# Kernel tuning notes

Hardware: AMD Instinct MI355X
Metric: run time of the kernel (lower is better)

## Reference

```python
import jax, jax.numpy as jnp
import numpy as np

B, L, C = 8, 2048, 512
R, H, DK = 256, 8, 64
MASK_NEG = -2.0**15 + 1.0


def setup_inputs() -> dict:
    key = jax.random.key(0)
    ks = jax.random.split(key, 9)
    s = 1.0 / np.sqrt(C)
    return {
        "qx": jax.random.normal(ks[0], (B, L, C), jnp.float32),
        "kx": jax.random.normal(ks[1], (B, L, C), jnp.float32),
        "vx": jax.random.normal(ks[2], (B, L, C), jnp.float32),
        "addLoss": jnp.zeros((), jnp.float32),
        "maskPAD": jnp.ones((B, L, L), jnp.bool_),
        "Wp": jax.random.normal(ks[3], (R, C), jnp.float32) * s,
        "WQ": jax.random.normal(ks[4], (H * DK, C), jnp.float32) * s,
        "WK": jax.random.normal(ks[5], (H * DK, C), jnp.float32) * s,
        "WV": jax.random.normal(ks[6], (H * DK, C), jnp.float32) * s,
        "WO": jax.random.normal(ks[7], (C, H * DK), jnp.float32) * (1.0 / np.sqrt(H * DK)),
    }


def reference(qx, kx, vx, addLoss, maskPAD, Wp, WQ, WK, WV, WO):
    # linearLevel == 'l1', dropout treated as identity (eval), training losses included
    b, l, c = qx.shape
    r = Wp.shape[0]
    offI = (1.0 - jnp.eye(r, dtype=qx.dtype))  # ones_minus_I, [r, r]

    pScore = jnp.einsum('blc,rc->blr', vx, Wp)                       # [B, L, r]
    pad = (maskPAD[:, 0] == 0)                                       # [B, L]
    pScore = jnp.where(pad[:, :, None], MASK_NEG, pScore)
    pAlpha = jnp.swapaxes(jax.nn.softmax(pScore, axis=-2), -1, -2)   # [B, r, L]
    pAlpha_ = jax.nn.softmax(pScore, axis=-1)                        # [B, L, r]

    addLoss = addLoss + jnp.mean((jnp.einsum('brl,bsl->brs', pAlpha, pAlpha) * offI) ** 2)

    qr = pAlpha @ qx                                                 # [B, r, C]
    kr = pAlpha @ kx
    vr = pAlpha @ vx

    queries = (qr @ WQ.T).reshape(b, r, H, DK).transpose(0, 2, 1, 3)  # [B, H, r, dk]
    keys = (kr @ WK.T).reshape(b, r, H, DK).transpose(0, 2, 1, 3)
    values = (vr @ WV.T).reshape(b, r, H, DK).transpose(0, 2, 1, 3)

    scores = jnp.einsum('bhrd,bhsd->bhrs', queries, keys) / jnp.asarray(np.sqrt(DK), qx.dtype)
    alpha = jax.nn.softmax(scores, axis=-1)                          # [B, H, r, r]
    addLoss = addLoss + jnp.mean(alpha * offI)

    z = alpha @ values                                               # [B, H, r, dk]
    z = z.transpose(0, 2, 1, 3).reshape(b, r, H * DK)
    z = z @ WO.T                                                     # [B, r, C]

    addLoss = addLoss + jnp.mean((jnp.einsum('blr,bls->brs', pAlpha_, pAlpha_) * offI) ** 2)
    z = pAlpha_ @ z                                                  # [B, L, C]
    return z, scores, addLoss
```

## Files before the change

### kernel.cpp

```cpp
#include <hip/hip_runtime.h>

#define B_  8
#define L_  2048
#define C_  512
#define R_  256
#define H_  8
#define DK_ 64
#define HD_ 512
#define MASK_NEG (-32767.0f)

typedef __attribute__((ext_vector_type(8))) short short8;
typedef __attribute__((ext_vector_type(8))) unsigned short ushort8;
typedef __attribute__((ext_vector_type(4))) unsigned short ushort4_t;
typedef __attribute__((ext_vector_type(4))) float f32x4;
typedef unsigned short u16;

__device__ inline u16 bf16_rne(float x) {
    unsigned u = __float_as_uint(x);
    return (u16)((u + 0x7FFFu + ((u >> 16) & 1u)) >> 16);
}
__device__ inline unsigned cvt_hl(float x) {
    u16 hh = bf16_rne(x);
    float hf = __uint_as_float(((unsigned)hh) << 16);
    u16 ll = bf16_rne(x - hf);
    return (unsigned)hh | ((unsigned)ll << 16);
}

struct Ptr3 { const void* p0; const void* p1; const void* p2; };

#define GLL16(g, l) __builtin_amdgcn_global_load_lds( \
    (const __attribute__((address_space(1))) void*)(g), \
    (__attribute__((address_space(3))) void*)(l), 16, 0, 0)

template<int BN, int AMODE, int BMODE, int EPI, bool TRIPLE, int NTERM = 3, int KSPLIT = 1>
__global__ __launch_bounds__(256) void gemm_pl(
    Ptr3 aH, Ptr3 aL, Ptr3 bH, Ptr3 bL, Ptr3 cH, Ptr3 cL,
    int K, int lda, int ldb, int ldc, int divz,
    long long ash, long long bsh, long long csh,
    long long asb, long long bsb, long long csb,
    long long ksa, long long ksb, long long ksc,
    float scale)
{
    constexpr int NF = BN / 32;
    constexpr int XA = (NTERM == 3) ? 64 : 1;
    constexpr int XB = (NTERM == 3) ? BN : 1;
    __shared__ u16 Ahs[64][40], Als[XA][40];
    __shared__ u16 Bhs[BN][40], Bls[XB][40];

    const int z  = blockIdx.z;
    const int zb = z / divz;
    const int rem = z - zb * divz;
    const int zh = rem / KSPLIT, ks = rem - zh * KSPLIT;
    const int Keff = K / KSPLIT;
    const void* avH = TRIPLE ? (zb == 0 ? aH.p0 : zb == 1 ? aH.p1 : aH.p2) : aH.p0;
    const void* avL = TRIPLE ? (zb == 0 ? aL.p0 : zb == 1 ? aL.p1 : aL.p2) : aL.p0;
    const void* bvH = TRIPLE ? (zb == 0 ? bH.p0 : zb == 1 ? bH.p1 : bH.p2) : bH.p0;
    const void* bvL = TRIPLE ? (zb == 0 ? bL.p0 : zb == 1 ? bL.p1 : bL.p2) : bL.p0;
    void* cvH = (void*)(TRIPLE ? (zb == 0 ? cH.p0 : zb == 1 ? cH.p1 : cH.p2) : cH.p0);
    void* cvL = (void*)(TRIPLE ? (zb == 0 ? cL.p0 : zb == 1 ? cL.p1 : cL.p2) : cL.p0);
    const long long ao = (TRIPLE ? 0 : (long long)zb * asb) + (long long)zh * ash + (long long)ks * ksa;
    const long long bo = (TRIPLE ? 0 : (long long)zb * bsb) + (long long)zh * bsh + (long long)ks * ksb;
    const long long co = (TRIPLE ? 0 : (long long)zb * csb) + (long long)zh * csh + (long long)ks * ksc;

    const u16*   AHg = (const u16*)avH + ao;
    const u16*   ALg = (const u16*)avL + ao;
    const u16*   BHg = (const u16*)bvH + bo;
    const u16*   BLg = (const u16*)bvL + bo;
    const float* Bfg = (const float*)bvH + bo;
    float* Cf  = (float*)cvH + co;
    u16*   CHg = (u16*)cvH + co;
    u16*   CLg = (u16*)cvL + co;

    const int m0 = blockIdx.y * 64, n0 = blockIdx.x * BN;
    const int tid = threadIdx.x;
    const int lane = tid & 63, w = tid >> 6;
    const int wrow = (w >> 1) * 32, wcol = (w & 1) * (BN / 2);
    const int l15 = lane & 15, lg = lane >> 4;

    f32x4 zero = {0.f, 0.f, 0.f, 0.f};
    f32x4 acc[2][NF];
    #pragma unroll
    for (int mf = 0; mf < 2; ++mf)
        #pragma unroll
        for (int nf = 0; nf < NF; ++nf) acc[mf][nf] = zero;

    for (int k0 = 0; k0 < Keff; k0 += 32) {
        {
            int row = tid >> 2, kc = (tid & 3) << 3;
            long long off = (long long)(m0 + row) * lda + (k0 + kc);
            *(ushort8*)&Ahs[row][kc] = *(const ushort8*)(AHg + off);
            if constexpr (NTERM == 3)
                *(ushort8*)&Als[row][kc] = *(const ushort8*)(ALg + off);
        }
        if (BMODE == 0) {
            #pragma unroll
            for (int t = tid; t < BN * 4; t += 256) {
                int row = t >> 2, kc = (t & 3) << 3;
                long long off = (long long)(n0 + row) * ldb + (k0 + kc);
                *(ushort8*)&Bhs[row][kc] = *(const ushort8*)(BHg + off);
                if constexpr (NTERM == 3)
                    *(ushort8*)&Bls[row][kc] = *(const ushort8*)(BLg + off);
            }
        } else {
            #pragma unroll
            for (int t = tid; t < BN * 4; t += 256) {
                int row = t >> 2, kc = (t & 3) << 3;
                const float* s = Bfg + (long long)(n0 + row) * ldb + (k0 + kc);
                float4 v0 = *(const float4*)s, v1 = *(const float4*)(s + 4);
                unsigned p0 = cvt_hl(v0.x), p1 = cvt_hl(v0.y), p2 = cvt_hl(v0.z), p3 = cvt_hl(v0.w);
                unsigned p4 = cvt_hl(v1.x), p5 = cvt_hl(v1.y), p6 = cvt_hl(v1.z), p7 = cvt_hl(v1.w);
                ushort8 h, l;
                h[0]=(u16)p0; h[1]=(u16)p1; h[2]=(u16)p2; h[3]=(u16)p3;
                h[4]=(u16)p4; h[5]=(u16)p5; h[6]=(u16)p6; h[7]=(u16)p7;
                l[0]=(u16)(p0>>16); l[1]=(u16)(p1>>16); l[2]=(u16)(p2>>16); l[3]=(u16)(p3>>16);
                l[4]=(u16)(p4>>16); l[5]=(u16)(p5>>16); l[6]=(u16)(p6>>16); l[7]=(u16)(p7>>16);
                *(ushort8*)&Bhs[row][kc] = h;
                if constexpr (NTERM == 3)
                    *(ushort8*)&Bls[row][kc] = l;
            }
        }
        __syncthreads();

        short8 a_h[2], a_l[2];
        a_h[0] = *(const short8*)&Ahs[wrow +      l15][lg * 8];
        a_h[1] = *(const short8*)&Ahs[wrow + 16 + l15][lg * 8];
        if constexpr (NTERM == 3) {
            a_l[0] = *(const short8*)&Als[wrow +      l15][lg * 8];
            a_l[1] = *(const short8*)&Als[wrow + 16 + l15][lg * 8];
        }
        #pragma unroll
        for (int nf = 0; nf < NF; ++nf) {
            short8 b_h = *(const short8*)&Bhs[wcol + nf * 16 + l15][lg * 8];
            if constexpr (NTERM == 3) {
                short8 b_l = *(const short8*)&Bls[wcol + nf * 16 + l15][lg * 8];
                #pragma unroll
                for (int mf = 0; mf < 2; ++mf) {
                    acc[mf][nf] = __builtin_amdgcn_mfma_f32_16x16x32_bf16(a_h[mf], b_h, acc[mf][nf], 0, 0, 0);
                    acc[mf][nf] = __builtin_amdgcn_mfma_f32_16x16x32_bf16(a_h[mf], b_l, acc[mf][nf], 0, 0, 0);
                    acc[mf][nf] = __builtin_amdgcn_mfma_f32_16x16x32_bf16(a_l[mf], b_h, acc[mf][nf], 0, 0, 0);
                }
            } else {
                #pragma unroll
                for (int mf = 0; mf < 2; ++mf)
                    acc[mf][nf] = __builtin_amdgcn_mfma_f32_16x16x32_bf16(a_h[mf], b_h, acc[mf][nf], 0, 0, 0);
            }
        }
        __syncthreads();
    }

    if (EPI == 0) {
        #pragma unroll
        for (int mf = 0; mf < 2; ++mf)
            #pragma unroll
            for (int nf = 0; nf < NF; ++nf) {
                int row = m0 + wrow + mf * 16 + lg * 4;
                int col = n0 + wcol + nf * 16 + l15;
                #pragma unroll
                for (int j = 0; j < 4; ++j)
                    Cf[(long long)(row + j) * ldc + col] = acc[mf][nf][j] * scale;
            }
    } else {
        #pragma unroll
        for (int mf = 0; mf < 2; ++mf)
            #pragma unroll
            for (int nf = 0; nf < NF; ++nf) {
                int row = m0 + wrow + mf * 16 + lg * 4;
                int col = n0 + wcol + nf * 16 + l15;
                #pragma unroll
                for (int j = 0; j < 4; ++j) {
                    unsigned p = cvt_hl(acc[mf][nf][j] * scale);
                    CHg[(long long)(row + j) * ldc + col] = (u16)p;
                    CLg[(long long)(row + j) * ldc + col] = (u16)(p >> 16);
                }
            }
    }
}

template<int EPI, bool TRIPLE, int NTERM, int KSPLIT>
__global__ __launch_bounds__(256) void gemm_gll(
    Ptr3 aH, Ptr3 aL, Ptr3 bH, Ptr3 bL, Ptr3 cH, Ptr3 cL,
    int K, int lda, int ldb, int ldc, int divz,
    long long ash, long long bsh, long long csh,
    long long ksa, long long ksb, long long ksc,
    float scale)
{
    constexpr int XA = (NTERM == 3) ? 128 : 1;
    __shared__ u16 Ahs[2][128][32];
    __shared__ u16 Bhs[2][128][32];
    __shared__ u16 Als[XA][32], Bls[XA][32];

    const int gx = gridDim.x, gy = gridDim.y;
    const int nwg = gx * gy * gridDim.z;
    int flat = blockIdx.x + gx * (blockIdx.y + gy * blockIdx.z);
    {
        int q = nwg >> 3;
        int xcd = flat & 7, idx = flat >> 3;
        flat = xcd * q + idx;
    }
    const int bx = flat % gx;
    const int by = (flat / gx) % gy;
    const int z  = flat / (gx * gy);

    const int zb = z / divz;
    const int rem = z - zb * divz;
    const int zh = rem / KSPLIT, ks = rem - zh * KSPLIT;
    const int Keff = K / KSPLIT;
    const void* avH = TRIPLE ? (zb == 0 ? aH.p0 : zb == 1 ? aH.p1 : aH.p2) : aH.p0;
    const void* avL = TRIPLE ? (zb == 0 ? aL.p0 : zb == 1 ? aL.p1 : aL.p2) : aL.p0;
    const void* bvH = TRIPLE ? (zb == 0 ? bH.p0 : zb == 1 ? bH.p1 : bH.p2) : bH.p0;
    const void* bvL = TRIPLE ? (zb == 0 ? bL.p0 : zb == 1 ? bL.p1 : bL.p2) : bL.p0;
    void* cvH = (void*)(TRIPLE ? (zb == 0 ? cH.p0 : zb == 1 ? cH.p1 : cH.p2) : cH.p0);
    void* cvL = (void*)(TRIPLE ? (zb == 0 ? cL.p0 : zb == 1 ? cL.p1 : cL.p2) : cL.p0);
    const long long ao = (long long)zh * ash + (long long)ks * ksa;
    const long long bo = (long long)zh * bsh + (long long)ks * ksb;
    const long long co = (long long)zh * csh + (long long)ks * ksc;

    const u16* AHg = (const u16*)avH + ao;
    const u16* ALg = (const u16*)avL + ao;
    const u16* BHg = (const u16*)bvH + bo;
    const u16* BLg = (const u16*)bvL + bo;
    float* Cf  = (float*)cvH + co;
    u16*   CHg = (u16*)cvH + co;
    u16*   CLg = (u16*)cvL + co;

    const int m0 = by * 128, n0 = bx * 128;
    const int tid = threadIdx.x;
    const int lane = tid & 63, w = tid >> 6;
    const int wrow = (w >> 1) * 64, wcol = (w & 1) * 64;
    const int l15 = lane & 15, lg = lane >> 4;

    f32x4 zero = {0.f, 0.f, 0.f, 0.f};
    f32x4 acc[4][4];
    #pragma unroll
    for (int mf = 0; mf < 4; ++mf)
        #pragma unroll
        for (int nf = 0; nf < 4; ++nf) acc[mf][nf] = zero;

    const int ric = lane >> 2;
    const int cc  = lane & 3;

    auto STAGE_HI = [&](int bufsel, int k0) {
        #pragma unroll
        for (int i = 0; i < 2; ++i) {
            int chunk = w * 2 + i;
            int row = chunk * 16 + ric;
            int gcol = ((cc ^ ((row >> 1) & 3)) << 3);
            GLL16(AHg + (long long)(m0 + row) * lda + (k0 + gcol), &Ahs[bufsel][chunk * 16][0]);
            GLL16(BHg + (long long)(n0 + row) * ldb + (k0 + gcol), &Bhs[bufsel][chunk * 16][0]);
        }
    };
    auto STAGE_LO = [&](int k0) {
        #pragma unroll
        for (int i = 0; i < 2; ++i) {
            int chunk = w * 2 + i;
            int row = chunk * 16 + ric;
            int gcol = ((cc ^ ((row >> 1) & 3)) << 3);
            GLL16(ALg + (long long)(m0 + row) * lda + (k0 + gcol), &Als[chunk * 16][0]);
            GLL16(BLg + (long long)(n0 + row) * ldb + (k0 + gcol), &Bls[chunk * 16][0]);
        }
    };

    const int nt = Keff / 32;
    int cur = 0;
    STAGE_HI(0, 0);

    for (int t = 0; t < nt; ++t) {
        if constexpr (NTERM == 3) STAGE_LO(t * 32);
        if (t + 1 < nt) {
            STAGE_HI(cur ^ 1, (t + 1) * 32);
            asm volatile("s_waitcnt vmcnt(4)" ::: "memory");
        } else {
            asm volatile("s_waitcnt vmcnt(0)" ::: "memory");
        }
        __builtin_amdgcn_s_barrier();

        short8 a_h[4], a_l[4];
        #pragma unroll
        for (int mf = 0; mf < 4; ++mf) {
            int ar = wrow + mf * 16 + l15;
            int ac = (lg ^ ((ar >> 1) & 3)) << 3;
            a_h[mf] = *(const short8*)&Ahs[cur][ar][ac];
            if constexpr (NTERM == 3) a_l[mf] = *(const short8*)&Als[ar][ac];
        }
        __builtin_amdgcn_s_setprio(1);
        #pragma unroll
        for (int nf = 0; nf < 4; ++nf) {
            int br = wcol + nf * 16 + l15;
            int bc = (lg ^ ((br >> 1) & 3)) << 3;
            short8 b_h = *(const short8*)&Bhs[cur][br][bc];
            if constexpr (NTERM == 3) {
                short8 b_l = *(const short8*)&Bls[br][bc];
                #pragma unroll
                for (int mf = 0; mf < 4; ++mf) {
                    acc[mf][nf] = __builtin_amdgcn_mfma_f32_16x16x32_bf16(a_h[mf], b_h, acc[mf][nf], 0, 0, 0);
                    acc[mf][nf] = __builtin_amdgcn_mfma_f32_16x16x32_bf16(a_h[mf], b_l, acc[mf][nf], 0, 0, 0);
                    acc[mf][nf] = __builtin_amdgcn_mfma_f32_16x16x32_bf16(a_l[mf], b_h, acc[mf][nf], 0, 0, 0);
                }
            } else {
                #pragma unroll
                for (int mf = 0; mf < 4; ++mf)
                    acc[mf][nf] = __builtin_amdgcn_mfma_f32_16x16x32_bf16(a_h[mf], b_h, acc[mf][nf], 0, 0, 0);
            }
        }
        __builtin_amdgcn_s_setprio(0);
        __builtin_amdgcn_s_barrier();
        cur ^= 1;
    }

    if (EPI == 0) {
        #pragma unroll
        for (int mf = 0; mf < 4; ++mf)
            #pragma unroll
            for (int nf = 0; nf < 4; ++nf) {
                int row = m0 + wrow + mf * 16 + lg * 4;
                int col = n0 + wcol + nf * 16 + l15;
                #pragma unroll
                for (int j = 0; j < 4; ++j)
                    Cf[(long long)(row + j) * ldc + col] = acc[mf][nf][j] * scale;
            }
    } else {
        #pragma unroll
        for (int mf = 0; mf < 4; ++mf)
            #pragma unroll
            for (int nf = 0; nf < 4; ++nf) {
                int row = m0 + wrow + mf * 16 + lg * 4;
                int col = n0 + wcol + nf * 16 + l15;
                #pragma unroll
                for (int j = 0; j < 4; ++j) {
                    unsigned p = cvt_hl(acc[mf][nf][j] * scale);
                    CHg[(long long)(row + j) * ldc + col] = (u16)p;
                    CLg[(long long)(row + j) * ldc + col] = (u16)(p >> 16);
                }
            }
    }
}

#define KS_ 4
__global__ __launch_bounds__(256) void loss_reduce(
    const float* __restrict__ G, int nks, float* __restrict__ lossDst)
{
    __shared__ float red[4];
    const long long N = (long long)B_ * R_ * R_;
    long long i4 = ((long long)blockIdx.x * 256 + threadIdx.x) << 2;
    float s = 0.0f;
    if (i4 < N) {
        float4 g = make_float4(0.f, 0.f, 0.f, 0.f);
        for (int ks = 0; ks < nks; ++ks) {
            float4 v = *(const float4*)(G + (long long)ks * N + i4);
            g.x += v.x; g.y += v.y; g.z += v.z; g.w += v.w;
        }
        int e = (int)(i4 & (long long)(R_ * R_ - 1));
        int row = e >> 8, c0 = e & 255;
        if (row != c0 + 0) s += g.x * g.x;
        if (row != c0 + 1) s += g.y * g.y;
        if (row != c0 + 2) s += g.z * g.z;
        if (row != c0 + 3) s += g.w * g.w;
    }
    #pragma unroll
    for (int o = 32; o; o >>= 1) s += __shfl_down(s, o, 64);
    int lane = threadIdx.x & 63, wid = threadIdx.x >> 6;
    if (lane == 0) red[wid] = s;
    __syncthreads();
    if (threadIdx.x == 0) atomicAdd(lossDst, red[0] + red[1] + red[2] + red[3]);
}

#define NKS6_ 2
__global__ __launch_bounds__(256) void qkv_reduce(
    const float* __restrict__ Cpart, Ptr3 dstH, Ptr3 dstL)
{
    const long long T = (long long)B_ * R_ * C_;
    long long i4 = (long long)blockIdx.x * 256 + threadIdx.x;
    if (i4 >= 3 * (T >> 2)) return;
    int member = (int)(i4 / (T >> 2));
    long long rem = (i4 - (long long)member * (T >> 2)) << 2;
    float4 a = *(const float4*)(Cpart + (long long)member * T + rem);
    #pragma unroll
    for (int ks = 1; ks < NKS6_; ++ks) {
        float4 b = *(const float4*)(Cpart + (long long)ks * 3 * T + (long long)member * T + rem);
        a.x += b.x; a.y += b.y; a.z += b.z; a.w += b.w;
    }
    unsigned q0 = cvt_hl(a.x), q1 = cvt_hl(a.y), q2 = cvt_hl(a.z), q3 = cvt_hl(a.w);
    ushort4_t h, l;
    h[0]=(u16)q0; h[1]=(u16)q1; h[2]=(u16)q2; h[3]=(u16)q3;
    l[0]=(u16)(q0>>16); l[1]=(u16)(q1>>16); l[2]=(u16)(q2>>16); l[3]=(u16)(q3>>16);
    u16* dH = (u16*)(member == 0 ? dstH.p0 : member == 1 ? dstH.p1 : dstH.p2);
    u16* dL = (u16*)(member == 0 ? dstL.p0 : member == 1 ? dstL.p1 : dstL.p2);
    *(ushort4_t*)(dH + rem) = h;
    *(ushort4_t*)(dL + rem) = l;
}

__global__ __launch_bounds__(256) void xpose_f32(
    const float* __restrict__ in, float* __restrict__ out,
    int M, int N, long long ibs, long long obs)
{
    __shared__ float S[64][65];
    const float* ip = in + (long long)blockIdx.z * ibs;
    float* op = out + (long long)blockIdx.z * obs;
    int n0 = blockIdx.x * 64, m0 = blockIdx.y * 64;
    int t = threadIdx.x;
    int c4 = (t & 15) << 2, rq = t >> 4;
    #pragma unroll
    for (int p = 0; p < 4; ++p) {
        int r = p * 16 + rq;
        float4 v = *(const float4*)(ip + (long long)(m0 + r) * N + n0 + c4);
        S[r][c4+0]=v.x; S[r][c4+1]=v.y; S[r][c4+2]=v.z; S[r][c4+3]=v.w;
    }
    __syncthreads();
    #pragma unroll
    for (int p = 0; p < 4; ++p) {
        int nr = p * 16 + rq;
        float4 o;
        o.x = S[c4+0][nr]; o.y = S[c4+1][nr]; o.z = S[c4+2][nr]; o.w = S[c4+3][nr];
        *(float4*)(op + (long long)(n0 + nr) * M + m0 + c4) = o;
    }
}

__global__ __launch_bounds__(256) void xpose_f32p3(
    Ptr3 src, Ptr3 dstH, Ptr3 dstL,
    int M, int N, long long ibs, long long obs, int divz)
{
    __shared__ float S[64][65];
    int z = blockIdx.z;
    int m = z / divz, b = z - m * divz;
    const float* ip = (const float*)(m == 0 ? src.p0 : m == 1 ? src.p1 : src.p2)
                      + (long long)b * ibs;
    u16* opH = (u16*)(m == 0 ? dstH.p0 : m == 1 ? dstH.p1 : dstH.p2) + (long long)b * obs;
    u16* opL = (u16*)(m == 0 ? dstL.p0 : m == 1 ? dstL.p1 : dstL.p2) + (long long)b * obs;
    int n0 = blockIdx.x * 64, m0 = blockIdx.y * 64;
    int t = threadIdx.x;
    int c4 = (t & 15) << 2, rq = t >> 4;
    #pragma unroll
    for (int p = 0; p < 4; ++p) {
        int r = p * 16 + rq;
        float4 v = *(const float4*)(ip + (long long)(m0 + r) * N + n0 + c4);
        S[r][c4+0]=v.x; S[r][c4+1]=v.y; S[r][c4+2]=v.z; S[r][c4+3]=v.w;
    }
    __syncthreads();
    #pragma unroll
    for (int p = 0; p < 4; ++p) {
        int nr = p * 16 + rq;
        unsigned q0 = cvt_hl(S[c4+0][nr]), q1 = cvt_hl(S[c4+1][nr]);
        unsigned q2 = cvt_hl(S[c4+2][nr]), q3 = cvt_hl(S[c4+3][nr]);
        ushort4_t h, l;
        h[0]=(u16)q0; h[1]=(u16)q1; h[2]=(u16)q2; h[3]=(u16)q3;
        l[0]=(u16)(q0>>16); l[1]=(u16)(q1>>16); l[2]=(u16)(q2>>16); l[3]=(u16)(q3>>16);
        long long ob = (long long)(n0 + nr) * M + m0 + c4;
        *(ushort4_t*)(opH + ob) = h;
        *(ushort4_t*)(opL + ob) = l;
    }
}

__global__ __launch_bounds__(256) void xpose_u16p(
    const u16* __restrict__ inH, const u16* __restrict__ inL,
    u16* __restrict__ outH, u16* __restrict__ outL,
    int M, int N, long long ibs, long long obs)
{
    __shared__ u16 SH[64][66], SL[64][66];
    const u16* ipH = inH + (long long)blockIdx.z * ibs;
    const u16* ipL = inL + (long long)blockIdx.z * ibs;
    u16* opH = outH + (long long)blockIdx.z * obs;
    u16* opL = outL + (long long)blockIdx.z * obs;
    int n0 = blockIdx.x * 64, m0 = blockIdx.y * 64;
    int t = threadIdx.x;
    int c4 = (t & 15) << 2, rq = t >> 4;
    #pragma unroll
    for (int p = 0; p < 4; ++p) {
        int r = p * 16 + rq;
        long long ib = (long long)(m0 + r) * N + n0 + c4;
        ushort4_t vh = *(const ushort4_t*)(ipH + ib);
        ushort4_t vl = *(const ushort4_t*)(ipL + ib);
        SH[r][c4+0]=vh[0]; SH[r][c4+1]=vh[1]; SH[r][c4+2]=vh[2]; SH[r][c4+3]=vh[3];
        SL[r][c4+0]=vl[0]; SL[r][c4+1]=vl[1]; SL[r][c4+2]=vl[2]; SL[r][c4+3]=vl[3];
    }
    __syncthreads();
    #pragma unroll
    for (int p = 0; p < 4; ++p) {
        int nr = p * 16 + rq;
        ushort4_t h, l;
        h[0]=SH[c4+0][nr]; h[1]=SH[c4+1][nr]; h[2]=SH[c4+2][nr]; h[3]=SH[c4+3][nr];
        l[0]=SL[c4+0][nr]; l[1]=SL[c4+1][nr]; l[2]=SL[c4+2][nr]; l[3]=SL[c4+3][nr];
        long long ob = (long long)(n0 + nr) * M + m0 + c4;
        *(ushort4_t*)(opH + ob) = h;
        *(ushort4_t*)(opL + ob) = l;
    }
}

__device__ inline float waveMax(float v) {
    #pragma unroll
    for (int o = 32; o; o >>= 1) v = fmaxf(v, __shfl_xor(v, o, 64));
    return v;
}
__device__ inline float waveSum(float v) {
    #pragma unroll
    for (int o = 32; o; o >>= 1) v += __shfl_xor(v, o, 64);
    return v;
}

__global__ __launch_bounds__(256) void conv_planes(
    const float* __restrict__ src, u16* __restrict__ h, u16* __restrict__ l, int n4)
{
    int i = blockIdx.x * 256 + threadIdx.x;
    if (i >= n4) return;
    float4 v = ((const float4*)src)[i];
    unsigned p0 = cvt_hl(v.x), p1 = cvt_hl(v.y), p2 = cvt_hl(v.z), p3 = cvt_hl(v.w);
    ushort4_t hv, lv;
    hv[0]=(u16)p0; hv[1]=(u16)p1; hv[2]=(u16)p2; hv[3]=(u16)p3;
    lv[0]=(u16)(p0>>16); lv[1]=(u16)(p1>>16); lv[2]=(u16)(p2>>16); lv[3]=(u16)(p3>>16);
    ((ushort4_t*)h)[i] = hv;
    ((ushort4_t*)l)[i] = lv;
}

__global__ __launch_bounds__(256) void softmax_LT(
    const float* __restrict__ pT, const int* __restrict__ mask,
    u16* __restrict__ outH, u16* __restrict__ outL)
{
    __shared__ float sm[4], ss[4];
    int zi = blockIdx.x;
    int b = zi >> 8;
    const float* row = pT + (long long)zi * L_;
    const int* mk = mask + (long long)b * L_ * L_;
    float vals[8];
    float mx = -3.4e38f;
    #pragma unroll
    for (int i = 0; i < 8; ++i) {
        int l = threadIdx.x + i * 256;
        float v = row[l];
        if (mk[l] == 0) v = MASK_NEG;
        vals[i] = v; mx = fmaxf(mx, v);
    }
    int lane = threadIdx.x & 63, wid = threadIdx.x >> 6;
    mx = waveMax(mx);
    if (lane == 0) sm[wid] = mx;
    __syncthreads();
    mx = fmaxf(fmaxf(sm[0], sm[1]), fmaxf(sm[2], sm[3]));
    float sum = 0.0f;
    #pragma unroll
    for (int i = 0; i < 8; ++i) { float e = __expf(vals[i] - mx); vals[i] = e; sum += e; }
    sum = waveSum(sum);
    if (lane == 0) ss[wid] = sum;
    __syncthreads();
    sum = ss[0] + ss[1] + ss[2] + ss[3];
    float inv = 1.0f / sum;
    long long base = (long long)zi * L_;
    #pragma unroll
    for (int i = 0; i < 8; ++i) {
        unsigned p = cvt_hl(vals[i] * inv);
        outH[base + threadIdx.x + i * 256] = (u16)p;
        outL[base + threadIdx.x + i * 256] = (u16)(p >> 16);
    }
}

__global__ __launch_bounds__(256) void softmax_R(
    const float* __restrict__ pScore, const int* __restrict__ mask,
    u16* __restrict__ outH, u16* __restrict__ outL)
{
    __shared__ float sm[4], ss[4];
    long long z = blockIdx.x;
    int b = (int)(z >> 11), l = (int)(z & 2047);
    bool pad = (mask[(long long)b * L_ * L_ + l] == 0);
    float v = pScore[z * R_ + threadIdx.x];
    if (pad) v = MASK_NEG;
    int lane = threadIdx.x & 63, wid = threadIdx.x >> 6;
    float mx = waveMax(v);
    if (lane == 0) sm[wid] = mx;
    __syncthreads();
    mx = fmaxf(fmaxf(sm[0], sm[1]), fmaxf(sm[2], sm[3]));
    float e = __expf(v - mx);
    float sum = waveSum(e);
    if (lane == 0) ss[wid] = sum;
    __syncthreads();
    sum = ss[0] + ss[1] + ss[2] + ss[3];
    unsigned p = cvt_hl(e / sum);
    outH[z * R_ + threadIdx.x] = (u16)p;
    outL[z * R_ + threadIdx.x] = (u16)(p >> 16);
}

__global__ __launch_bounds__(256) void softmax_alpha(
    const float* __restrict__ scores, u16* __restrict__ aH, u16* __restrict__ aL,
    float* __restrict__ offArr)
{
    __shared__ float sm[4], ss[4], so[4];
    long long row = blockIdx.x;
    int r = (int)(row & 255);
    float v = scores[row * 256 + threadIdx.x];
    int lane = threadIdx.x & 63, wid = threadIdx.x >> 6;
    float mx = waveMax(v);
    if (lane == 0) sm[wid] = mx;
    __syncthreads();
    mx = fmaxf(fmaxf(sm[0], sm[1]), fmaxf(sm[2], sm[3]));
    float e = __expf(v - mx);
    float sum = waveSum(e);
    if (lane == 0) ss[wid] = sum;
    __syncthreads();
    sum = ss[0] + ss[1] + ss[2] + ss[3];
    float a = e / sum;
    unsigned p = cvt_hl(a);
    aH[row * 256 + threadIdx.x] = (u16)p;
    aL[row * 256 + threadIdx.x] = (u16)(p >> 16);
    float off = (threadIdx.x == r) ? 0.0f : a;
    off = waveSum(off);
    if (lane == 0) so[wid] = off;
    __syncthreads();
    if (threadIdx.x == 0) offArr[row] = so[0] + so[1] + so[2] + so[3];
}

__global__ __launch_bounds__(256) void finalize_loss(
    const float* __restrict__ addLossIn, const float* __restrict__ lossAcc,
    const float* __restrict__ offArr, float* __restrict__ out)
{
    __shared__ float red[4];
    float s = 0.0f;
    for (int i = threadIdx.x; i < B_ * H_ * R_; i += 256) s += offArr[i];
    int lane = threadIdx.x & 63, wid = threadIdx.x >> 6;
    s = waveSum(s);
    if (lane == 0) red[wid] = s;
    __syncthreads();
    if (threadIdx.x == 0) {
        float total = red[0] + red[1] + red[2] + red[3];
        out[0] = addLossIn[0]
               + lossAcc[0] * (1.0f / ((float)B_ * R_ * R_))
               + total      * (1.0f / ((float)B_ * H_ * R_ * R_))
               + lossAcc[2] * (1.0f / ((float)B_ * R_ * R_));
    }
}

extern "C" void kernel_launch(void* const* d_in, const int* in_sizes, int n_in,
                              void* d_out, int out_size, void* d_ws, size_t ws_size,
                              hipStream_t stream)
{
    const float* qx = (const float*)d_in[0];
    const float* kx = (const float*)d_in[1];
    const float* vx = (const float*)d_in[2];
    const float* addLossIn = (const float*)d_in[3];
    const int* mask = (const int*)d_in[4];
    const float* Wp = (const float*)d_in[5];
    const float* WQ = (const float*)d_in[6];
    const float* WK = (const float*)d_in[7];
    const float* WV = (const float*)d_in[8];
    const float* WO = (const float*)d_in[9];

    float* zOut      = (float*)d_out;
    float* scoresOut = zOut + (long long)B_ * L_ * C_;
    float* lossOut   = scoresOut + (long long)B_ * H_ * R_ * R_;

    const long long S = (long long)B_ * L_ * R_;
    const long long T = (long long)B_ * R_ * C_;
    u16* cur = (u16*)d_ws;
    auto takeU = [&](long long n) { u16* p = cur; cur += n; return p; };
    auto takeF = [&](long long n) { float* p = (float*)cur; cur += 2 * n; return p; };

    float* pScore   = takeF(S);
    float* pScoreT  = takeF(S);
    u16* pAlphaH  = takeU(S);
    u16* pAlphaL  = takeU(S);
    u16* pAlpha_H = takeU(S);
    u16* pAlpha_L = takeU(S);
    u16* pATH     = takeU(S);
    u16* pATL     = takeU(S);
    u16* xTH0 = takeU(2*S); u16* xTL0 = takeU(2*S);
    u16* xTH1 = takeU(2*S); u16* xTL1 = takeU(2*S);
    u16* xTH2 = takeU(2*S); u16* xTL2 = takeU(2*S);
    const long long llRR = (long long)R_ * R_;
    float* Gpart  = takeF(2LL * KS_ * B_ * llRR);
    float* Cpart6 = takeF((long long)NKS6_ * 3 * T);
    u16* qrH = takeU(T); u16* qrL = takeU(T);
    u16* krH = takeU(T); u16* krL = takeU(T);
    u16* vrH = takeU(T); u16* vrL = takeU(T);
    u16* qpH = takeU(T); u16* qpL = takeU(T);
    u16* kpH = takeU(T); u16* kpL = takeU(T);
    u16* vpH = takeU(T); u16* vpL = takeU(T);
    u16* vpTH = takeU(T); u16* vpTL = takeU(T);
    u16* z1H = takeU(T); u16* z1L = takeU(T);
    u16* z2H = takeU(T); u16* z2L = takeU(T);
    u16* z2TH = takeU(T); u16* z2TL = takeU(T);
    u16* alphaH = takeU(S); u16* alphaL = takeU(S);
    u16* WpH = takeU((long long)R_ * C_); u16* WpL = takeU((long long)R_ * C_);
    u16* WQH = takeU((long long)HD_ * C_); u16* WQL = takeU((long long)HD_ * C_);
    u16* WKH = takeU((long long)HD_ * C_); u16* WKL = takeU((long long)HD_ * C_);
    u16* WVH = takeU((long long)HD_ * C_); u16* WVL = takeU((long long)HD_ * C_);
    u16* WOH = takeU((long long)HD_ * C_); u16* WOL = takeU((long long)HD_ * C_);
    float* loss   = takeF(16);
    float* offArr = takeF(B_ * H_ * R_);

    const Ptr3 N3{nullptr, nullptr, nullptr};
    auto P1 = [](const void* p) { return Ptr3{p, p, p}; };
    const long long llRL = (long long)R_ * L_, llLC = (long long)L_ * C_;
    const long long llRC = (long long)R_ * C_, llRHD = (long long)R_ * HD_;
    const long long llHRR = (long long)H_ * R_ * R_;
    const long long llCL = (long long)C_ * L_;
    float* Gpart2 = Gpart + (long long)KS_ * B_ * llRR;

    (void)hipMemsetAsync(loss, 0, 3 * sizeof(float), stream);

    conv_planes<<<(R_*C_/4 + 255)/256, 256, 0, stream>>>(Wp, WpH, WpL, R_*C_/4);
    conv_planes<<<(HD_*C_/4 + 255)/256, 256, 0, stream>>>(WQ, WQH, WQL, HD_*C_/4);
    conv_planes<<<(HD_*C_/4 + 255)/256, 256, 0, stream>>>(WK, WKH, WKL, HD_*C_/4);
    conv_planes<<<(HD_*C_/4 + 255)/256, 256, 0, stream>>>(WV, WVH, WVL, HD_*C_/4);
    conv_planes<<<(HD_*C_/4 + 255)/256, 256, 0, stream>>>(WO, WOH, WOL, HD_*C_/4);

    gemm_pl<64, 0, 2, 0, false><<<dim3(L_/64, R_/64, B_), 256, 0, stream>>>(
        P1(WpH), P1(WpL), P1(vx), N3, P1(pScoreT), N3,
        C_, C_, C_, L_, B_,
        0, llLC, llRL, 0, 0, 0, 0, 0, 0, 1.0f);

    xpose_f32<<<dim3(L_/64, R_/64, B_), 256, 0, stream>>>(
        pScoreT, pScore, R_, L_, llRL, llRL);

    softmax_LT<<<B_ * R_, 256, 0, stream>>>(pScoreT, mask, pAlphaH, pAlphaL);
    softmax_R<<<B_ * L_, 256, 0, stream>>>(pScore, mask, pAlpha_H, pAlpha_L);

    xpose_u16p<<<dim3(R_/64, L_/64, B_), 256, 0, stream>>>(
        pAlpha_H, pAlpha_L, pATH, pATL, L_, R_, llRL, llRL);

    gemm_gll<0, true, 1, KS_><<<dim3(2, 2, 2 * B_ * KS_), 256, 0, stream>>>(
        Ptr3{pAlphaH, pATH, pATH}, N3, Ptr3{pAlphaH, pATH, pATH}, N3,
        Ptr3{Gpart, Gpart2, Gpart2}, N3,
        L_, L_, L_, R_, B_ * KS_,
        llRL, llRL, llRR,
        L_ / KS_, L_ / KS_, (long long)B_ * llRR, 1.0f);
    loss_reduce<<<512, 256, 0, stream>>>(Gpart, KS_, loss + 0);
    loss_reduce<<<512, 256, 0, stream>>>(Gpart2, KS_, loss + 2);

    xpose_f32p3<<<dim3(C_/64, L_/64, 3 * B_), 256, 0, stream>>>(
        Ptr3{qx, kx, vx}, Ptr3{xTH0, xTH1, xTH2}, Ptr3{xTL0, xTL1, xTL2},
        L_, C_, llLC, llCL, B_);

    gemm_gll<0, true, 3, NKS6_><<<dim3(C_/128, R_/128, 3 * B_ * NKS6_), 256, 0, stream>>>(
        P1(pAlphaH), P1(pAlphaL),
        Ptr3{xTH0, xTH1, xTH2}, Ptr3{xTL0, xTL1, xTL2},
        Ptr3{Cpart6, Cpart6 + T, Cpart6 + 2 * T}, N3,
        L_, L_, L_, C_, B_ * NKS6_,
        llRL, llCL, llRC,
        L_ / NKS6_, L_ / NKS6_, 3 * T, 1.0f);

    qkv_reduce<<<(int)(3 * (T >> 2) / 256), 256, 0, stream>>>(
        Cpart6, Ptr3{qrH, krH, vrH}, Ptr3{qrL, krL, vrL});

    gemm_gll<2, true, 3, 1><<<dim3(HD_/128, 16, 3), 256, 0, stream>>>(
        Ptr3{qrH, krH, vrH}, Ptr3{qrL, krL, vrL},
        Ptr3{WQH, WKH, WVH}, Ptr3{WQL, WKL, WVL},
        Ptr3{qpH, kpH, vpH}, Ptr3{qpL, kpL, vpL},
        C_, C_, C_, HD_, 1,
        0, 0, 0, 0, 0, 0, 1.0f);

    xpose_u16p<<<dim3(HD_/64, R_/64, B_), 256, 0, stream>>>(
        vpH, vpL, vpTH, vpTL, R_, HD_, llRHD, llRHD);

    gemm_pl<64, 0, 0, 0, false><<<dim3(4, 4, 64), 256, 0, stream>>>(
        P1(qpH), P1(qpL), P1(kpH), P1(kpL), P1(scoresOut), N3,
        DK_, HD_, HD_, R_, 8, 64, 64, llRR, llRHD, llRHD, llHRR,
        0, 0, 0, 0.125f);

    softmax_alpha<<<B_ * H_ * R_, 256, 0, stream>>>(scoresOut, alphaH, alphaL, offArr);

    gemm_pl<64, 0, 0, 2, false><<<dim3(1, 4, 64), 256, 0, stream>>>(
        P1(alphaH), P1(alphaL), P1(vpTH), P1(vpTL), P1(z1H), P1(z1L),
        R_, R_, R_, HD_, 8, llRR, (long long)64 * R_, 64, llHRR, llRHD, llRHD,
        0, 0, 0, 1.0f);

    gemm_pl<64, 0, 0, 2, false><<<dim3(8, 32, 1), 256, 0, stream>>>(
        P1(z1H), P1(z1L), P1(WOH), P1(WOL), P1(z2H), P1(z2L),
        HD_, HD_, HD_, C_, 1, 0, 0, 0, 0, 0, 0, 0, 0, 0, 1.0f);

    xpose_u16p<<<dim3(C_/64, R_/64, B_), 256, 0, stream>>>(
        z2H, z2L, z2TH, z2TL, R_, C_, llRC, llRC);

    gemm_gll<0, false, 3, 1><<<dim3(C_/128, L_/128, B_), 256, 0, stream>>>(
        P1(pAlpha_H), P1(pAlpha_L), P1(z2TH), P1(z2TL), P1(zOut), N3,
        R_, R_, R_, C_, B_,
        llRL, llRC, llLC,
        0, 0, 0, 1.0f);

    finalize_loss<<<1, 256, 0, stream>>>(addLossIn, loss, offArr, lossOut);
}
```

Baseline: 349.3 us.

## Remap gemm_pl workgroups by XCD and merge weight conversions into one launch

The gemm_pl kernel now remaps the flat workgroup index so that consecutive logical tiles land on the same XCD (chiplet-aware swizzle across 8 XCDs), aiming to improve L2 reuse of shared operand tiles. Separately, the five per-weight bf16 hi/lo conversion launches are merged into one kernel covering all segments, reducing launch overhead. The swizzle assumes the total workgroup count is divisible by 8; otherwise the mapping would drop or duplicate tiles.

```diff
diff --git a/kernel.cpp b/kernel.cpp
--- a/kernel.cpp
+++ b/kernel.cpp
@@ -47,7 +47,18 @@
     __shared__ u16 Ahs[64][40], Als[XA][40];
     __shared__ u16 Bhs[BN][40], Bls[XB][40];
 
-    const int z  = blockIdx.z;
+    const int gx = gridDim.x, gy = gridDim.y;
+    const int nwg = gx * gy * gridDim.z;
+    int flat = blockIdx.x + gx * (blockIdx.y + gy * blockIdx.z);
+    {
+        int q = nwg >> 3;
+        int xcd = flat & 7, idx = flat >> 3;
+        flat = xcd * q + idx;
+    }
+    const int bx = flat % gx;
+    const int by = (flat / gx) % gy;
+    const int z  = flat / (gx * gy);
+
     const int zb = z / divz;
     const int rem = z - zb * divz;
     const int zh = rem / KSPLIT, ks = rem - zh * KSPLIT;
@@ -71,7 +82,7 @@
     u16*   CHg = (u16*)cvH + co;
     u16*   CLg = (u16*)cvL + co;
 
-    const int m0 = blockIdx.y * 64, n0 = blockIdx.x * BN;
+    const int m0 = by * 64, n0 = bx * BN;
     const int tid = threadIdx.x;
     const int lane = tid & 63, w = tid >> 6;
     const int wrow = (w >> 1) * 32, wcol = (w & 1) * (BN / 2);
@@ -496,18 +507,31 @@
     return v;
 }
 
-__global__ __launch_bounds__(256) void conv_planes(
-    const float* __restrict__ src, u16* __restrict__ h, u16* __restrict__ l, int n4)
-{
+__global__ __launch_bounds__(256) void conv_planes5(
+    const float* __restrict__ s0, const float* __restrict__ s1, const float* __restrict__ s2,
+    const float* __restrict__ s3, const float* __restrict__ s4,
+    u16* h0, u16* l0, u16* h1, u16* l1, u16* h2, u16* l2,
+    u16* h3, u16* l3, u16* h4, u16* l4)
+{
+    const int N0 = 32768, NW = 65536;
     int i = blockIdx.x * 256 + threadIdx.x;
-    if (i >= n4) return;
-    float4 v = ((const float4*)src)[i];
+    if (i >= N0 + 4 * NW) return;
+    const float* s; u16* h; u16* l; int off;
+    if (i < N0) { s = s0; h = h0; l = l0; off = i; }
+    else {
+        int j = i - N0, seg = j / NW;
+        off = j - seg * NW;
+        s = seg == 0 ? s1 : seg == 1 ? s2 : seg == 2 ? s3 : s4;
+        h = seg == 0 ? h1 : seg == 1 ? h2 : seg == 2 ? h3 : h4;
+        l = seg == 0 ? l1 : seg == 1 ? l2 : seg == 2 ? l3 : l4;
+    }
+    float4 v = ((const float4*)s)[off];
     unsigned p0 = cvt_hl(v.x), p1 = cvt_hl(v.y), p2 = cvt_hl(v.z), p3 = cvt_hl(v.w);
     ushort4_t hv, lv;
     hv[0]=(u16)p0; hv[1]=(u16)p1; hv[2]=(u16)p2; hv[3]=(u16)p3;
     lv[0]=(u16)(p0>>16); lv[1]=(u16)(p1>>16); lv[2]=(u16)(p2>>16); lv[3]=(u16)(p3>>16);
-    ((ushort4_t*)h)[i] = hv;
-    ((ushort4_t*)l)[i] = lv;
+    ((ushort4_t*)h)[off] = hv;
+    ((ushort4_t*)l)[off] = lv;
 }
 
 __global__ __launch_bounds__(256) void softmax_LT(
@@ -692,11 +716,9 @@
 
     (void)hipMemsetAsync(loss, 0, 3 * sizeof(float), stream);
 
-    conv_planes<<<(R_*C_/4 + 255)/256, 256, 0, stream>>>(Wp, WpH, WpL, R_*C_/4);
-    conv_planes<<<(HD_*C_/4 + 255)/256, 256, 0, stream>>>(WQ, WQH, WQL, HD_*C_/4);
-    conv_planes<<<(HD_*C_/4 + 255)/256, 256, 0, stream>>>(WK, WKH, WKL, HD_*C_/4);
-    conv_planes<<<(HD_*C_/4 + 255)/256, 256, 0, stream>>>(WV, WVH, WVL, HD_*C_/4);
-    conv_planes<<<(HD_*C_/4 + 255)/256, 256, 0, stream>>>(WO, WOH, WOL, HD_*C_/4);
+    conv_planes5<<<1152, 256, 0, stream>>>(
+        Wp, WQ, WK, WV, WO,
+        WpH, WpL, WQH, WQL, WKH, WKL, WVH, WVL, WOH, WOL);
 
     gemm_pl<64, 0, 2, 0, false><<<dim3(L_/64, R_/64, B_), 256, 0, stream>>>(
         P1(WpH), P1(WpL), P1(vx), N3, P1(pScoreT), N3,
```

After: 336.8 us. 3.6% less time.
